# Performance work log

Measured on AMD Instinct MI355X. Metric: run time of the kernel, lower is better.

The kernel has to match this reference:

```python
import jax, jax.numpy as jnp
import numpy as np

LEVELS = (1, 2, 4)
NHEAD = 4
LN_EPS = 1e-5


def _layernorm(x, g, b):
    m = jnp.mean(x, axis=-1, keepdims=True)
    v = jnp.mean((x - m) ** 2, axis=-1, keepdims=True)
    return (x - m) * jax.lax.rsqrt(v + LN_EPS) * g + b


def _spp_pool(x, starts, ends):
    # Exact AdaptiveAvgPool1d over per-proposal segments via inclusive-prefix-sum.
    # x: [B,C,T]; starts/ends: [B,P] int. Returns [B, P, C*sum(LEVELS)].
    B, C, T = x.shape
    P = starts.shape[1]
    xt = jnp.transpose(x, (0, 2, 1))  # [B,T,C]
    csum = jnp.concatenate([jnp.zeros((B, 1, C), x.dtype), jnp.cumsum(xt, axis=1)], axis=1)  # [B,T+1,C]
    n = ends - starts  # [B,P], always >= 1
    feats = []
    for L in LEVELS:
        i = jnp.arange(L)
        lo = (starts[..., None] + (i * n[..., None]) // L).reshape(B, P * L)
        hi = (starts[..., None] + ((i + 1) * n[..., None] + L - 1) // L).reshape(B, P * L)
        slo = jnp.take_along_axis(csum, lo[..., None], axis=1)  # [B,P*L,C]
        shi = jnp.take_along_axis(csum, hi[..., None], axis=1)
        mean = (shi - slo) / (hi - lo).astype(x.dtype)[..., None]
        # torch view(N, C*L) flattens [C,L] C-major -> transpose bins to last axis
        feats.append(mean.reshape(B, P, L, C).transpose(0, 1, 3, 2).reshape(B, P, C * L))
    return jnp.concatenate(feats, axis=-1)


def _encoder_layer(x, qkv_w, qkv_b, out_w, out_b, g1, b1, w1, bb1, w2, bb2, g2, b2):
    # Post-norm nn.TransformerEncoderLayer with exact-erf gelu, dropout=0 (eval)
    B, P, d = x.shape
    dh = d // NHEAD
    qkv = x @ qkv_w.T + qkv_b  # [B,P,3d]
    q, k, v = jnp.split(qkv, 3, axis=-1)
    sh = lambda t: t.reshape(B, P, NHEAD, dh).transpose(0, 2, 1, 3)  # [B,H,P,dh]
    q, k, v = sh(q), sh(k), sh(v)
    scale = 1.0 / float(np.sqrt(dh))
    attn = jax.nn.softmax(jnp.einsum('bhqd,bhkd->bhqk', q, k) * scale, axis=-1)
    o = jnp.einsum('bhqk,bhkd->bhqd', attn, v).transpose(0, 2, 1, 3).reshape(B, P, d)
    o = o @ out_w.T + out_b
    x = _layernorm(x + o, g1, b1)
    h = jax.nn.gelu(x @ w1.T + bb1, approximate=False) @ w2.T + bb2
    return _layernorm(x + h, g2, b2)


def _forward(x, proposal_boxes, proj_w, proj_b, pos_w1, pos_b1, pos_w2, pos_b2,
             qkv_w, qkv_b, out_w, out_b, ln1_g, ln1_b, ff1_w, ff1_b,
             ff2_w, ff2_b, ln2_g, ln2_b, cls_w, cls_b, det_w, det_b):
    B, C, T = x.shape
    P = proposal_boxes.shape[1]
    starts = jnp.clip(proposal_boxes[..., 0], 0, T - 1)
    ends = jnp.clip(proposal_boxes[..., 1], 1, T)
    ends = jnp.where(ends <= starts, jnp.minimum(starts + 1, T), ends)
    feats = _spp_pool(x, starts, ends)  # [B,P,spp_out_dim]
    s_f = proposal_boxes[..., 0].astype(x.dtype)
    e_f = proposal_boxes[..., 1].astype(x.dtype)
    centers = (s_f + e_f) / 2.0
    lengths = jnp.maximum(e_f - s_f, 1.0)
    pos_feat = jnp.stack([centers / T, lengths / T], axis=-1)  # [B,P,2]
    sort_idx = jnp.argsort(centers, axis=1)
    feats_s = jnp.take_along_axis(feats, sort_idx[..., None], axis=1)
    pos_emb = jax.nn.relu(pos_feat @ pos_w1.T + pos_b1) @ pos_w2.T + pos_b2
    pos_emb_s = jnp.take_along_axis(pos_emb, sort_idx[..., None], axis=1)
    tok = feats_s @ proj_w.T + proj_b + pos_emb_s  # [B,P,d]
    for l in range(qkv_w.shape[0]):
        tok = _encoder_layer(tok, qkv_w[l], qkv_b[l], out_w[l], out_b[l],
                             ln1_g[l], ln1_b[l], ff1_w[l], ff1_b[l],
                             ff2_w[l], ff2_b[l], ln2_g[l], ln2_b[l])
    inv = jnp.argsort(sort_idx, axis=1)
    ctx = jnp.take_along_axis(tok, inv[..., None], axis=1)  # [B,P,d]
    class_logits = ctx @ cls_w.T + cls_b  # [B,P,nc]
    det_logits = ctx @ det_w.T + det_b
    class_prob = jax.nn.softmax(class_logits, axis=2)
    det_prob = jax.nn.softmax(det_logits, axis=1)
    joint_prob = class_prob * det_prob
    video_prob = joint_prob.sum(axis=1)
    return video_prob, joint_prob, class_logits, det_logits, ctx


def setup_inputs() -> dict:
    key = jax.random.key(0)
    ks = jax.random.split(key, 32)
    B, C, T, P = 8, 512, 2048, 512
    d, dff, nc, nl = 512, 1024, 30, 2
    spp_out = C * sum(LEVELS)
    s = 0.02
    f32 = jnp.float32
    inp = {
        'x': jax.random.normal(ks[0], (B, C, T), f32),
        'proposal_boxes': jax.random.randint(ks[1], (B, P, 2), 0, T).astype(jnp.int32),
        'proj_w': jax.random.normal(ks[2], (d, spp_out), f32) * s,
        'proj_b': jnp.zeros((d,), f32),
        'pos_w1': jax.random.normal(ks[3], (d, 2), f32) * s,
        'pos_b1': jnp.zeros((d,), f32),
        'pos_w2': jax.random.normal(ks[4], (d, d), f32) * s,
        'pos_b2': jnp.zeros((d,), f32),
        'qkv_w': jax.random.normal(ks[5], (nl, 3 * d, d), f32) * s,
        'qkv_b': jnp.zeros((nl, 3 * d), f32),
        'out_w': jax.random.normal(ks[6], (nl, d, d), f32) * s,
        'out_b': jnp.zeros((nl, d), f32),
        'ln1_g': jnp.ones((nl, d), f32),
        'ln1_b': jnp.zeros((nl, d), f32),
        'ff1_w': jax.random.normal(ks[7], (nl, dff, d), f32) * s,
        'ff1_b': jnp.zeros((nl, dff), f32),
        'ff2_w': jax.random.normal(ks[8], (nl, d, dff), f32) * s,
        'ff2_b': jnp.zeros((nl, d), f32),
        'ln2_g': jnp.ones((nl, d), f32),
        'ln2_b': jnp.zeros((nl, d), f32),
        'cls_w': jax.random.normal(ks[9], (nc, d), f32) * s,
        'cls_b': jnp.zeros((nc,), f32),
        'det_w': jax.random.normal(ks[10], (nc, d), f32) * s,
        'det_b': jnp.zeros((nc,), f32),
    }
    return inp


def reference(x, proposal_boxes, proj_w, proj_b, pos_w1, pos_b1, pos_w2, pos_b2,
              qkv_w, qkv_b, out_w, out_b, ln1_g, ln1_b, ff1_w, ff1_b,
              ff2_w, ff2_b, ln2_g, ln2_b, cls_w, cls_b, det_w, det_b):
    return _forward(x, proposal_boxes, proj_w, proj_b, pos_w1, pos_b1, pos_w2, pos_b2,
                    qkv_w, qkv_b, out_w, out_b, ln1_g, ln1_b, ff1_w, ff1_b,
                    ff2_w, ff2_b, ln2_g, ln2_b, cls_w, cls_b, det_w, det_b)
```

## Files before the change

kernel.cpp:

```cpp
#include <hip/hip_runtime.h>

#define TDIM 2048
#define CDIM 512
#define BDIM 8
#define PDIM 512
#define DMODEL 512
#define NCOUT 30
#define SPPOUT 3584
#define AKDIM 4096

typedef __attribute__((ext_vector_type(8))) short short8;
typedef __attribute__((ext_vector_type(4))) float f32x4;

typedef const __attribute__((address_space(1))) void* as1cv;
typedef __attribute__((address_space(3))) void* as3v;

__device__ __forceinline__ void gl_lds16(const short* g, short* l){
  __builtin_amdgcn_global_load_lds((as1cv)g, (as3v)l, 16, 0, 0);
}

__device__ __forceinline__ short f2b(float f){
  unsigned u = __float_as_uint(f);
  unsigned r = (u + 0x7fffu + ((u >> 16) & 1u)) >> 16;
  return (short)r;
}

__device__ __forceinline__ float waveSum(float v){
#pragma unroll
  for (int o = 32; o > 0; o >>= 1) v += __shfl_xor(v, o);
  return v;
}
__device__ __forceinline__ float waveMax(float v){
#pragma unroll
  for (int o = 32; o > 0; o >>= 1) v = fmaxf(v, __shfl_xor(v, o));
  return v;
}

__global__ void kprep2(const float* __restrict__ pw, const float* __restrict__ pw2,
                       const float* __restrict__ qw, const float* __restrict__ ow,
                       const float* __restrict__ f1, const float* __restrict__ f2,
                       const float* __restrict__ cl, const float* __restrict__ dt,
                       const float* __restrict__ pb, const float* __restrict__ pb2,
                       const float* __restrict__ cb, const float* __restrict__ db,
                       short* __restrict__ Wc, short* __restrict__ Wd,
                       float* __restrict__ bc, float* __restrict__ bh){
  int i = blockIdx.x * 256 + threadIdx.x;
  if (i < 2097152){
    int r = i >> 12, k = i & 4095;
    float v = (k < SPPOUT) ? pw[(size_t)r * SPPOUT + k] : pw2[(size_t)r * DMODEL + (k - SPPOUT)];
    Wc[i] = f2b(v);
  } else if (i < 6322176){
    int j = i - 2097152;
    float v;
    if (j < 1572864) v = qw[j];
    else if (j < 2097152) v = ow[j - 1572864];
    else if (j < 3145728) v = f1[j - 2097152];
    else if (j < 4194304) v = f2[j - 3145728];
    else if (j < 4209664) v = cl[j - 4194304];
    else v = dt[j - 4209664];
    Wd[j] = f2b(v);
  } else {
    int k = i - 6322176;
    if (k < 512) bc[k] = pb[k] + pb2[k];
    else if (k < 572) bh[k - 512] = (k < 542) ? cb[k - 512] : db[k - 542];
  }
}

__global__ void kscan(const float* __restrict__ x, float* __restrict__ W, float* __restrict__ tot){
  int idx = blockIdx.x;
  int b = idx >> 5, rem = idx & 31, ch = rem >> 1, cg = rem & 1;
  int c = cg * 256 + threadIdx.x;
  const float* xp = x + ((size_t)(b * CDIM + c)) * TDIM + ch * 128;
  float* wp = W + ((size_t)b * TDIM + ch * 128) * CDIM + c;
  float run = 0.f;
  for (int tl = 0; tl < 128; tl += 4){
    float4 v = *(const float4*)(xp + tl);
    run += v.x; wp[(size_t)(tl + 0) * CDIM] = run;
    run += v.y; wp[(size_t)(tl + 1) * CDIM] = run;
    run += v.z; wp[(size_t)(tl + 2) * CDIM] = run;
    run += v.w; wp[(size_t)(tl + 3) * CDIM] = run;
  }
  tot[((size_t)b * 16 + ch) * CDIM + c] = run;
}

__global__ void koff(const float* __restrict__ tot, float* __restrict__ off){
  int b = blockIdx.x >> 1, cg = blockIdx.x & 1;
  int c = cg * 256 + threadIdx.x;
  float run = 0.f;
  for (int ch = 0; ch < 16; ++ch){
    off[((size_t)b * 16 + ch) * CDIM + c] = run;
    run += tot[((size_t)b * 16 + ch) * CDIM + c];
  }
}

__global__ void ksort(const int* __restrict__ boxes, int* __restrict__ sidx, float* __restrict__ out){
  __shared__ unsigned key[PDIM];
  int b = blockIdx.x, t = threadIdx.x;
  if (b == 0 && t < 240) out[t] = 0.f;
  int s = boxes[(size_t)(b * PDIM + t) * 2];
  int e = boxes[(size_t)(b * PDIM + t) * 2 + 1];
  key[t] = ((unsigned)(s + e) << 9) | (unsigned)t;
  __syncthreads();
  for (int k = 2; k <= PDIM; k <<= 1){
    for (int j = k >> 1; j > 0; j >>= 1){
      int ixj = t ^ j;
      if (ixj > t){
        unsigned a = key[t], c2 = key[ixj];
        bool up = ((t & k) == 0);
        bool doswap = up ? (a > c2) : (a < c2);
        if (doswap){ key[t] = c2; key[ixj] = a; }
      }
      __syncthreads();
    }
  }
  sidx[b * PDIM + t] = (int)(key[t] & 511u);
}

__global__ void kspp(const float* __restrict__ W, const float* __restrict__ off,
                     const int* __restrict__ boxes, const int* __restrict__ sidx,
                     const float* __restrict__ pw1, const float* __restrict__ pb1,
                     short* __restrict__ A){
  int blk = blockIdx.x;
  int b = blk >> 9, j = blk & 511;
  int p = sidx[b * PDIM + j];
  int s0 = boxes[(size_t)(b * PDIM + p) * 2];
  int e0 = boxes[(size_t)(b * PDIM + p) * 2 + 1];
  int start = min(max(s0, 0), TDIM - 1);
  int end   = min(max(e0, 1), TDIM);
  if (end <= start) end = min(start + 1, TDIM);
  int n = end - start;

  int lo[7], hi[7], cb[7], cl[7];
  {
    const int Ls[3] = {1, 2, 4};
    const int Bo[3] = {0, 512, 1536};
    int q = 0;
    for (int li = 0; li < 3; ++li){
      int L = Ls[li];
      for (int i = 0; i < L; ++i){
        lo[q] = start + (i * n) / L;
        hi[q] = start + ((i + 1) * n + L - 1) / L;
        cb[q] = Bo[li] + i;
        cl[q] = L;
        ++q;
      }
    }
  }
  float s_f = (float)s0, e_f = (float)e0;
  float px = (s_f + e_f) * 0.5f / (float)TDIM;
  float py = fmaxf(e_f - s_f, 1.f) / (float)TDIM;
  short* Ar = A + (size_t)(b * PDIM + j) * AKDIM;
  const float* Wb = W + (size_t)b * TDIM * CDIM;
  const float* ob = off + (size_t)b * 16 * CDIM;
  for (int c = threadIdx.x; c < CDIM; c += 256){
#pragma unroll
    for (int q = 0; q < 7; ++q){
      int l = lo[q], h = hi[q];
      float fl = (l == 0) ? 0.f : (Wb[(size_t)(l - 1) * CDIM + c] + ob[((l - 1) >> 7) * CDIM + c]);
      float fh = Wb[(size_t)(h - 1) * CDIM + c] + ob[((h - 1) >> 7) * CDIM + c];
      Ar[cb[q] + c * cl[q]] = f2b((fh - fl) / (float)(h - l));
    }
    float hv = pw1[c * 2] * px + pw1[c * 2 + 1] * py + pb1[c];
    Ar[SPPOUT + c] = f2b(fmaxf(hv, 0.f));
  }
}

template<int BN, int SWZ = 0>
__global__ __launch_bounds__(256) void gemm_bt(
    int M, int N, int K,
    const short* __restrict__ A, int lda, long long sAb, long long sAh,
    const short* __restrict__ B, int ldb, long long sBb, long long sBh,
    float* __restrict__ Cf, short* __restrict__ Cb, int ldc, long long sCb, long long sCh,
    int hdiv, float alpha,
    const float* __restrict__ bias, const float* __restrict__ resid, int act)
{
  constexpr int JF = BN / 32;
  __shared__ short As[128 * 64];
  __shared__ short Bs[BN * 64];
  int bx = blockIdx.x, by = blockIdx.y, bz = blockIdx.z;
  if constexpr (SWZ){
    int nx = gridDim.x, ny = gridDim.y;
    int rt = ny >> 3;
    int flat = (bz * ny + by) * nx + bx;
    int xcd = flat & 7, wl = flat >> 3;
    by = xcd * rt + wl % rt;
    int rest = wl / rt;
    bx = rest % nx;
    bz = rest / nx;
  }
  int zb = bz / hdiv, zh = bz - zb * hdiv;
  A += (size_t)zb * sAb + (size_t)zh * sAh;
  B += (size_t)zb * sBb + (size_t)zh * sBh;
  size_t coff = (size_t)zb * sCb + (size_t)zh * sCh;
  int rowBase = by * 128, colBase = bx * BN;
  int t = threadIdx.x;
  int lane = t & 63;
  int wave = t >> 6;
  int wm = (wave >> 1) * 64, wn = (wave & 1) * (BN / 2);
  int lm = lane & 15, quad = lane >> 4;
  int srow = t >> 3;
  int skw = ((t & 7) * 8) ^ ((srow & 7) * 8);

  const short* Agp[4];
#pragma unroll
  for (int it = 0; it < 4; ++it)
    Agp[it] = A + (size_t)min(rowBase + srow + it * 32, M - 1) * lda + skw;
  const short* Bgp[JF];
#pragma unroll
  for (int it = 0; it < JF; ++it)
    Bgp[it] = B + (size_t)min(colBase + srow + it * 32, N - 1) * ldb + skw;

  f32x4 zero4 = {0.f, 0.f, 0.f, 0.f};
  f32x4 acc[4][JF];
#pragma unroll
  for (int i = 0; i < 4; ++i)
#pragma unroll
    for (int j = 0; j < JF; ++j) acc[i][j] = zero4;

  int axr = (lm & 7) * 8;
  for (int k0 = 0; k0 < K; k0 += 64){
#pragma unroll
    for (int it = 0; it < 4; ++it) gl_lds16(Agp[it] + k0, As + it * 2048 + t * 8);
#pragma unroll
    for (int it = 0; it < JF; ++it) gl_lds16(Bgp[it] + k0, Bs + it * 2048 + t * 8);
    __syncthreads();
#pragma unroll
    for (int h = 0; h < 2; ++h){
      int koff = (h * 32 + quad * 8) ^ axr;
      short8 af[4], bfr[JF];
#pragma unroll
      for (int i = 0; i < 4; ++i)
        af[i] = *(const short8*)(As + (wm + i * 16 + lm) * 64 + koff);
#pragma unroll
      for (int j = 0; j < JF; ++j)
        bfr[j] = *(const short8*)(Bs + (wn + j * 16 + lm) * 64 + koff);
#pragma unroll
      for (int i = 0; i < 4; ++i)
#pragma unroll
        for (int j = 0; j < JF; ++j)
          acc[i][j] = __builtin_amdgcn_mfma_f32_16x16x32_bf16(af[i], bfr[j], acc[i][j], 0, 0, 0);
    }
    __syncthreads();
  }

#pragma unroll
  for (int i = 0; i < 4; ++i){
#pragma unroll
    for (int j = 0; j < JF; ++j){
#pragma unroll
      for (int r = 0; r < 4; ++r){
        int row = rowBase + wm + i * 16 + quad * 4 + r;
        int col = colBase + wn + j * 16 + lm;
        if (row < M && col < N){
          float v = acc[i][j][r] * alpha;
          if (bias) v += bias[col];
          size_t ci = coff + (size_t)row * ldc + col;
          if (resid) v += resid[ci];
          if (act) v = 0.5f * v * (1.f + erff(v * 0.7071067811865476f));
          if (Cf) Cf[ci] = v;
          if (Cb) Cb[ci] = f2b(v);
        }
      }
    }
  }
}

__global__ void kredG1(const float* __restrict__ part, const float* __restrict__ bias,
                       float* __restrict__ tok, short* __restrict__ tokb){
  int i = blockIdx.x * 256 + threadIdx.x;
  float v = part[i] + part[i + 2097152] + part[i + 4194304] + part[i + 6291456] + bias[i & 511];
  tok[i] = v;
  tokb[i] = f2b(v);
}

__global__ void kvt(const short* __restrict__ qkvb, short* __restrict__ Vt){
  __shared__ short T[32][33];
  int bh = blockIdx.x, pt = blockIdx.y, nt = blockIdx.z;
  int b = bh >> 2, h = bh & 3;
  int tx = threadIdx.x, ty = threadIdx.y;
  const short* src = qkvb + (size_t)(b * 512) * 1536 + 1024 + h * 128;
  int p0 = pt * 32, n0 = nt * 32;
#pragma unroll
  for (int q = 0; q < 4; ++q)
    T[ty * 4 + q][tx] = src[(size_t)(p0 + ty * 4 + q) * 1536 + n0 + tx];
  __syncthreads();
  short* dst = Vt + (size_t)bh * 128 * 512;
#pragma unroll
  for (int q = 0; q < 4; ++q)
    dst[(size_t)(n0 + ty * 4 + q) * 512 + p0 + tx] = T[tx][ty * 4 + q];
}

__global__ __launch_bounds__(256) void kflash(const short* __restrict__ qkvb,
                                              const short* __restrict__ Vt,
                                              short* __restrict__ ob){
  __shared__ float Ofs[4][16][128];
  __shared__ float Ml[4][16], Ll[4][16], Fw[4][16], Linv[16];
  int bid = blockIdx.x;
  int bh = bid & 31, qt = bid >> 5;
  int b = bh >> 2, h = bh & 3;
  int t = threadIdx.x;
  int w = t >> 6, lane = t & 63;
  int lm = lane & 15, quad = lane >> 4;
  const float SL2 = 0.1275174468f;

  const short* qbase = qkvb + (size_t)(b * 512 + qt * 16 + lm) * 1536 + h * 128 + quad * 8;
  short8 qf[4];
#pragma unroll
  for (int s = 0; s < 4; ++s) qf[s] = *(const short8*)(qbase + s * 32);

  const short* kbase = qkvb + (size_t)(b * 512) * 1536 + 512 + h * 128 + quad * 8;
  const short* vbase = Vt + (size_t)bh * 65536 + (size_t)lm * 512 + quad * 8;

  f32x4 zero4 = {0.f, 0.f, 0.f, 0.f};
  f32x4 Of[8];
#pragma unroll
  for (int i = 0; i < 8; ++i) Of[i] = zero4;
  float mrun[4] = {-1e30f, -1e30f, -1e30f, -1e30f};
  float lrun[4] = {0.f, 0.f, 0.f, 0.f};
  short* Pw = (short*)&Ofs[w][0][0];

#pragma unroll
  for (int kt = 0; kt < 2; ++kt){
    int kb = w * 128 + kt * 64;
    f32x4 Sf[4];
#pragma unroll
    for (int j = 0; j < 4; ++j) Sf[j] = zero4;
#pragma unroll
    for (int s = 0; s < 4; ++s){
#pragma unroll
      for (int j = 0; j < 4; ++j){
        short8 kf = *(const short8*)(kbase + (size_t)(kb + j * 16 + lm) * 1536 + s * 32);
        Sf[j] = __builtin_amdgcn_mfma_f32_16x16x32_bf16(qf[s], kf, Sf[j], 0, 0, 0);
      }
    }
    float alpha[4];
#pragma unroll
    for (int r = 0; r < 4; ++r){
      float mx = fmaxf(fmaxf(Sf[0][r], Sf[1][r]), fmaxf(Sf[2][r], Sf[3][r])) * SL2;
#pragma unroll
      for (int o = 1; o < 16; o <<= 1) mx = fmaxf(mx, __shfl_xor(mx, o));
      float mnew = fmaxf(mrun[r], mx);
      alpha[r] = exp2f(mrun[r] - mnew);
      float psum = 0.f;
#pragma unroll
      for (int j = 0; j < 4; ++j){
        float p = exp2f(Sf[j][r] * SL2 - mnew);
        Sf[j][r] = p;
        psum += p;
      }
#pragma unroll
      for (int o = 1; o < 16; o <<= 1) psum += __shfl_xor(psum, o);
      lrun[r] = lrun[r] * alpha[r] + psum;
      mrun[r] = mnew;
    }
#pragma unroll
    for (int i = 0; i < 8; ++i)
#pragma unroll
      for (int r = 0; r < 4; ++r) Of[i][r] *= alpha[r];
#pragma unroll
    for (int j = 0; j < 4; ++j)
#pragma unroll
      for (int r = 0; r < 4; ++r){
        int q = quad * 4 + r;
        int key = j * 16 + lm;
        Pw[q * 64 + (key ^ ((q & 7) * 8))] = f2b(Sf[j][r]);
      }
#pragma unroll
    for (int ts = 0; ts < 2; ++ts){
      short8 pa = *(const short8*)(Pw + lm * 64 + (((ts * 32 + quad * 8) ^ ((lm & 7) * 8))));
#pragma unroll
      for (int jd = 0; jd < 8; ++jd){
        short8 vf = *(const short8*)(vbase + (size_t)(jd * 16) * 512 + kb + ts * 32);
        Of[jd] = __builtin_amdgcn_mfma_f32_16x16x32_bf16(pa, vf, Of[jd], 0, 0, 0);
      }
    }
  }

#pragma unroll
  for (int jd = 0; jd < 8; ++jd)
#pragma unroll
    for (int r = 0; r < 4; ++r)
      Ofs[w][quad * 4 + r][jd * 16 + lm] = Of[jd][r];
  if (lm == 0){
#pragma unroll
    for (int r = 0; r < 4; ++r){
      Ml[w][quad * 4 + r] = mrun[r];
      Ll[w][quad * 4 + r] = lrun[r];
    }
  }
  __syncthreads();

  if (t < 64){
    int wv = t >> 4, row = t & 15;
    float M = fmaxf(fmaxf(Ml[0][row], Ml[1][row]), fmaxf(Ml[2][row], Ml[3][row]));
    Fw[wv][row] = exp2f(Ml[wv][row] - M);
    if (wv == 0){
      float lsum = Ll[0][row] * exp2f(Ml[0][row] - M) + Ll[1][row] * exp2f(Ml[1][row] - M)
                 + Ll[2][row] * exp2f(Ml[2][row] - M) + Ll[3][row] * exp2f(Ml[3][row] - M);
      Linv[row] = 1.f / lsum;
    }
  }
  __syncthreads();

  {
    int row = t >> 4, dbase = (t & 15) * 8;
    float f0 = Fw[0][row], f1 = Fw[1][row], f2v = Fw[2][row], f3 = Fw[3][row];
    float li = Linv[row];
    short* dst = ob + ((size_t)(b * 512 + qt * 16 + row)) * 512 + h * 128 + dbase;
#pragma unroll
    for (int u = 0; u < 8; ++u){
      float v = Ofs[0][row][dbase + u] * f0 + Ofs[1][row][dbase + u] * f1
              + Ofs[2][row][dbase + u] * f2v + Ofs[3][row][dbase + u] * f3;
      dst[u] = f2b(v * li);
    }
  }
}

__global__ void klnR(const float* __restrict__ part, const float* __restrict__ bias,
                     const float* __restrict__ resid,
                     const float* __restrict__ g, const float* __restrict__ bb,
                     float* __restrict__ Yf, short* __restrict__ Yb){
  int row = blockIdx.x, lane = threadIdx.x;
  size_t base = (size_t)row * DMODEL;
  float v[8]; float s = 0.f;
#pragma unroll
  for (int i = 0; i < 8; ++i){
    int c = lane + 64 * i;
    v[i] = part[base + c] + part[base + c + 2097152] + bias[c] + resid[base + c];
    s += v[i];
  }
  s = waveSum(s);
  float m = s * (1.f / DMODEL);
  float q = 0.f;
#pragma unroll
  for (int i = 0; i < 8; ++i){ float d = v[i] - m; q += d * d; }
  q = waveSum(q);
  float inv = rsqrtf(q * (1.f / DMODEL) + 1e-5f);
#pragma unroll
  for (int i = 0; i < 8; ++i){
    int c = lane + 64 * i;
    float o = (v[i] - m) * inv * g[c] + bb[c];
    Yf[base + c] = o;
    Yb[base + c] = f2b(o);
  }
}

__global__ void kdetsm(const float* __restrict__ hd, float* __restrict__ dp){
  int b = blockIdx.x / NCOUT, c = blockIdx.x % NCOUT, lane = threadIdx.x;
  float v[8]; float m = -1e30f;
#pragma unroll
  for (int i = 0; i < 8; ++i){
    v[i] = hd[((size_t)(b * PDIM) + lane + 64 * i) * 60 + 30 + c];
    m = fmaxf(m, v[i]);
  }
  m = waveMax(m);
  float s = 0.f;
#pragma unroll
  for (int i = 0; i < 8; ++i){ v[i] = expf(v[i] - m); s += v[i]; }
  s = waveSum(s);
  float r = 1.f / s;
#pragma unroll
  for (int i = 0; i < 8; ++i)
    dp[((size_t)(b * PDIM) + lane + 64 * i) * NCOUT + c] = v[i] * r;
}

__global__ void kfinal(const float* __restrict__ hd, const float* __restrict__ dps,
                       const float* __restrict__ tok, const int* __restrict__ sidx,
                       float* __restrict__ out){
  int blk = blockIdx.x;
  int b = blk >> 9, j = blk & 511;
  int lane = threadIdx.x;
  int p = sidx[b * PDIM + j];
  float* video = out;
  float* joint = out + 240;
  float* clso  = out + 123120;
  float* deto  = out + 246000;
  float* ctxo  = out + 368880;
  size_t rs60 = (size_t)(b * PDIM + j) * 60;
  size_t rs30 = (size_t)(b * PDIM + j) * NCOUT;
  size_t ro = (size_t)(b * PDIM + p) * NCOUT;
  float lc = (lane < NCOUT) ? hd[rs60 + lane] : -1e30f;
  float m = waveMax(lc);
  float e = (lane < NCOUT) ? expf(lc - m) : 0.f;
  float s = waveSum(e);
  float cp = e / s;
  if (lane < NCOUT){
    float dv  = hd[rs60 + 30 + lane];
    float dpv = dps[rs30 + lane];
    float jp  = cp * dpv;
    clso[ro + lane] = lc;
    deto[ro + lane] = dv;
    joint[ro + lane] = jp;
    atomicAdd(&video[b * NCOUT + lane], jp);
  }
  const float* tr = tok + (size_t)(b * PDIM + j) * DMODEL;
  float* cr = ctxo + (size_t)(b * PDIM + p) * DMODEL;
  for (int c = lane; c < DMODEL; c += 64) cr[c] = tr[c];
}

extern "C" void kernel_launch(void* const* d_in, const int* in_sizes, int n_in,
                              void* d_out, int out_size, void* d_ws, size_t ws_size,
                              hipStream_t stream) {
  const float* x      = (const float*)d_in[0];
  const int*   boxes  = (const int*)d_in[1];
  const float* proj_w = (const float*)d_in[2];
  const float* proj_b = (const float*)d_in[3];
  const float* pos_w1 = (const float*)d_in[4];
  const float* pos_b1 = (const float*)d_in[5];
  const float* pos_w2 = (const float*)d_in[6];
  const float* pos_b2 = (const float*)d_in[7];
  const float* qkv_w  = (const float*)d_in[8];
  const float* qkv_b  = (const float*)d_in[9];
  const float* out_w  = (const float*)d_in[10];
  const float* out_b  = (const float*)d_in[11];
  const float* ln1_g  = (const float*)d_in[12];
  const float* ln1_b  = (const float*)d_in[13];
  const float* ff1_w  = (const float*)d_in[14];
  const float* ff1_b  = (const float*)d_in[15];
  const float* ff2_w  = (const float*)d_in[16];
  const float* ff2_b  = (const float*)d_in[17];
  const float* ln2_g  = (const float*)d_in[18];
  const float* ln2_b  = (const float*)d_in[19];
  const float* cls_w  = (const float*)d_in[20];
  const float* cls_b  = (const float*)d_in[21];
  const float* det_w  = (const float*)d_in[22];
  const float* det_b  = (const float*)d_in[23];
  float* out = (float*)d_out;
  float* ws  = (float*)d_ws;

  const size_t oR1    = 0;
  const size_t oS     = 9437184;
  const size_t oTok   = 22020096;
  const size_t oTokb  = 24117248;
  const size_t oTok2  = 25165824;
  const size_t oTok2b = 27262976;
  const size_t oWcat  = 28311552;
  const size_t oBcat  = 29360128;
  const size_t oWq    = 29360640;
  const size_t oWo    = 30147072;
  const size_t oWf1   = 30409216;
  const size_t oWf2   = 30933504;
  const size_t oWcls  = 31457792;
  const size_t oTot   = 31473152;
  const size_t oOff   = 31538688;
  const size_t oSidx  = 31604224;
  const size_t oBhead = oTot;

  short* Abf   = (short*)(ws + oR1);
  short* qkvb  = (short*)(ws + oR1);
  short* Vt    = (short*)(ws + oR1 + 3145728);
  short* obufb = (short*)(ws + oR1 + 4194304);
  short* hbufb = (short*)(ws + oR1 + 5242880);
  float* headS = ws + oR1 + 7340032;
  float* dpS   = ws + oR1 + 7585792;
  float* csum  = ws + oS;
  float* Cpart = ws + oS;
  float* Cp2   = ws + oS;
  float* tok   = ws + oTok;
  short* tokb  = (short*)(ws + oTokb);
  float* tok2  = ws + oTok2;
  short* tok2b = (short*)(ws + oTok2b);
  short* Wcatb = (short*)(ws + oWcat);
  float* bcat  = ws + oBcat;
  short* Wq    = (short*)(ws + oWq);
  short* Wo    = (short*)(ws + oWo);
  short* Wf1   = (short*)(ws + oWf1);
  short* Wf2   = (short*)(ws + oWf2);
  short* Whead = (short*)(ws + oWcls);
  float* tot   = ws + oTot;
  float* offp  = ws + oOff;
  int*   sidx  = (int*)(ws + oSidx);
  float* bhead = ws + oBhead;

  kscan<<<256, 256, 0, stream>>>(x, csum, tot);
  koff<<<16, 256, 0, stream>>>(tot, offp);
  ksort<<<BDIM, 512, 0, stream>>>(boxes, sidx, out);
  kprep2<<<24699, 256, 0, stream>>>(proj_w, pos_w2, qkv_w, out_w, ff1_w, ff2_w, cls_w, det_w,
                                    proj_b, pos_b2, cls_b, det_b, Wcatb, Wq, bcat, bhead);
  kspp<<<BDIM * PDIM, 256, 0, stream>>>(csum, offp, boxes, sidx, pos_w1, pos_b1, Abf);

  gemm_bt<128, 1><<<dim3(4, 32, 4), 256, 0, stream>>>(
      4096, 512, 1024, Abf, 4096, 1024, 0, Wcatb, 4096, 1024, 0,
      Cpart, nullptr, 512, 2097152, 0, 1, 1.f, nullptr, nullptr, 0);
  kredG1<<<8192, 256, 0, stream>>>(Cpart, bcat, tok, tokb);

  for (int l = 0; l < 2; ++l){
    const short* qw  = Wq  + (size_t)l * 1536 * 512;
    const short* ow  = Wo  + (size_t)l * 512 * 512;
    const short* f1w = Wf1 + (size_t)l * 1024 * 512;
    const short* f2w = Wf2 + (size_t)l * 512 * 1024;
    const float* qb  = qkv_b + (size_t)l * 1536;
    const float* obv = out_b + (size_t)l * 512;
    const float* f1b = ff1_b + (size_t)l * 1024;
    const float* f2b_ = ff2_b + (size_t)l * 512;

    gemm_bt<128, 1><<<dim3(12, 32, 1), 256, 0, stream>>>(
        4096, 1536, 512, tokb, 512, 0, 0, qw, 512, 0, 0,
        nullptr, qkvb, 1536, 0, 0, 1, 1.f, qb, nullptr, 0);
    kvt<<<dim3(32, 16, 4), dim3(32, 8), 0, stream>>>(qkvb, Vt);
    kflash<<<1024, 256, 0, stream>>>(qkvb, Vt, obufb);
    gemm_bt<64><<<dim3(8, 32, 2), 256, 0, stream>>>(
        4096, 512, 256, obufb, 512, 256, 0, ow, 512, 256, 0,
        Cp2, nullptr, 512, 2097152, 0, 1, 1.f, nullptr, nullptr, 0);
    klnR<<<4096, 64, 0, stream>>>(Cp2, obv, tok, ln1_g + l * 512, ln1_b + l * 512, tok2, tok2b);
    gemm_bt<64><<<dim3(16, 32, 1), 256, 0, stream>>>(
        4096, 1024, 512, tok2b, 512, 0, 0, f1w, 512, 0, 0,
        nullptr, hbufb, 1024, 0, 0, 1, 1.f, f1b, nullptr, 1);
    gemm_bt<64><<<dim3(8, 32, 2), 256, 0, stream>>>(
        4096, 512, 512, hbufb, 1024, 512, 0, f2w, 1024, 512, 0,
        Cp2, nullptr, 512, 2097152, 0, 1, 1.f, nullptr, nullptr, 0);
    klnR<<<4096, 64, 0, stream>>>(Cp2, f2b_, tok2, ln2_g + l * 512, ln2_b + l * 512, tok, tokb);
  }

  gemm_bt<64><<<dim3(1, 32, 1), 256, 0, stream>>>(
      4096, 60, 512, tokb, 512, 0, 0, Whead, 512, 0, 0,
      headS, nullptr, 60, 0, 0, 1, 1.f, bhead, nullptr, 0);
  kdetsm<<<BDIM * NCOUT, 64, 0, stream>>>(headS, dpS);
  kfinal<<<BDIM * PDIM, 64, 0, stream>>>(headS, dpS, tok, sidx, out);
}
```

Before: 554.7 us.

## Fuse V transpose into QKV GEMM epilogue and widen split-K for projections

The QKV projection GEMM now writes the V part directly in transposed layout through an LDS staging tile in its epilogue, which removes the separate kvt transpose kernel. The out-projection and FF2 GEMMs go from 2-way to 4-way split-K, and the LayerNorm reduction kernel now sums four partial buffers. Several GEMMs switch to BN=64 tiles with more blocks to raise parallelism. The trade-off is more partial-sum traffic in the reduction kernels and an extra shared-memory pass in the V blocks.

Measured after the change: 522.6 us. 1.06x faster.

```diff
diff --git a/kernel.cpp b/kernel.cpp
--- a/kernel.cpp
+++ b/kernel.cpp
@@ -10,6 +10,7 @@
 #define AKDIM 4096
 
 typedef __attribute__((ext_vector_type(8))) short short8;
+typedef __attribute__((ext_vector_type(4))) short short4v;
 typedef __attribute__((ext_vector_type(4))) float f32x4;
 
 typedef const __attribute__((address_space(1))) void* as1cv;
@@ -172,11 +173,13 @@
     const short* __restrict__ B, int ldb, long long sBb, long long sBh,
     float* __restrict__ Cf, short* __restrict__ Cb, int ldc, long long sCb, long long sCh,
     int hdiv, float alpha,
-    const float* __restrict__ bias, const float* __restrict__ resid, int act)
+    const float* __restrict__ bias, const float* __restrict__ resid, int act,
+    short* __restrict__ Vtp)
 {
   constexpr int JF = BN / 32;
-  __shared__ short As[128 * 64];
-  __shared__ short Bs[BN * 64];
+  __shared__ short smem[128 * 64 + BN * 64];
+  short* As = smem;
+  short* Bs = smem + 128 * 64;
   int bx = blockIdx.x, by = blockIdx.y, bz = blockIdx.z;
   if constexpr (SWZ){
     int nx = gridDim.x, ny = gridDim.y;
@@ -243,6 +246,36 @@
     __syncthreads();
   }
 
+  if (Vtp && colBase >= 1024){
+    short* LT = smem;
+#pragma unroll
+    for (int i = 0; i < 4; ++i){
+#pragma unroll
+      for (int j = 0; j < JF; ++j){
+        int d = wn + j * 16 + lm;
+        int prow = wm + i * 16 + quad * 4;
+        short4v pk;
+#pragma unroll
+        for (int r = 0; r < 4; ++r){
+          float v = acc[i][j][r] * alpha;
+          if (bias) v += bias[colBase + d];
+          pk[r] = f2b(v);
+        }
+        *(short4v*)(LT + d * 132 + prow) = pk;
+      }
+    }
+    __syncthreads();
+    int bb = rowBase >> 9;
+    int hh = (colBase - 1024) >> 7;
+    int dd0 = (colBase - 1024) & 127;
+    int dl = t >> 2, pl = (t & 3) * 32;
+    const short* sp = LT + dl * 132 + pl;
+    short* dp = Vtp + ((size_t)(bb * 4 + hh)) * 65536 + (size_t)(dd0 + dl) * 512 + (rowBase & 511) + pl;
+#pragma unroll
+    for (int u = 0; u < 4; ++u) *(short8*)(dp + u * 8) = *(const short8*)(sp + u * 8);
+    return;
+  }
+
 #pragma unroll
   for (int i = 0; i < 4; ++i){
 #pragma unroll
@@ -273,23 +306,6 @@
   tokb[i] = f2b(v);
 }
 
-__global__ void kvt(const short* __restrict__ qkvb, short* __restrict__ Vt){
-  __shared__ short T[32][33];
-  int bh = blockIdx.x, pt = blockIdx.y, nt = blockIdx.z;
-  int b = bh >> 2, h = bh & 3;
-  int tx = threadIdx.x, ty = threadIdx.y;
-  const short* src = qkvb + (size_t)(b * 512) * 1536 + 1024 + h * 128;
-  int p0 = pt * 32, n0 = nt * 32;
-#pragma unroll
-  for (int q = 0; q < 4; ++q)
-    T[ty * 4 + q][tx] = src[(size_t)(p0 + ty * 4 + q) * 1536 + n0 + tx];
-  __syncthreads();
-  short* dst = Vt + (size_t)bh * 128 * 512;
-#pragma unroll
-  for (int q = 0; q < 4; ++q)
-    dst[(size_t)(n0 + ty * 4 + q) * 512 + p0 + tx] = T[tx][ty * 4 + q];
-}
-
 __global__ __launch_bounds__(256) void kflash(const short* __restrict__ qkvb,
                                               const short* __restrict__ Vt,
                                               short* __restrict__ ob){
@@ -426,7 +442,8 @@
 #pragma unroll
   for (int i = 0; i < 8; ++i){
     int c = lane + 64 * i;
-    v[i] = part[base + c] + part[base + c + 2097152] + bias[c] + resid[base + c];
+    v[i] = part[base + c] + part[base + c + 2097152] + part[base + c + 4194304]
+         + part[base + c + 6291456] + bias[c] + resid[base + c];
     s += v[i];
   }
   s = waveSum(s);
@@ -579,9 +596,9 @@
                                     proj_b, pos_b2, cls_b, det_b, Wcatb, Wq, bcat, bhead);
   kspp<<<BDIM * PDIM, 256, 0, stream>>>(csum, offp, boxes, sidx, pos_w1, pos_b1, Abf);
 
-  gemm_bt<128, 1><<<dim3(4, 32, 4), 256, 0, stream>>>(
+  gemm_bt<64, 1><<<dim3(8, 32, 4), 256, 0, stream>>>(
       4096, 512, 1024, Abf, 4096, 1024, 0, Wcatb, 4096, 1024, 0,
-      Cpart, nullptr, 512, 2097152, 0, 1, 1.f, nullptr, nullptr, 0);
+      Cpart, nullptr, 512, 2097152, 0, 1, 1.f, nullptr, nullptr, 0, nullptr);
   kredG1<<<8192, 256, 0, stream>>>(Cpart, bcat, tok, tokb);
 
   for (int l = 0; l < 2; ++l){
@@ -594,27 +611,26 @@
     const float* f1b = ff1_b + (size_t)l * 1024;
     const float* f2b_ = ff2_b + (size_t)l * 512;
 
-    gemm_bt<128, 1><<<dim3(12, 32, 1), 256, 0, stream>>>(
+    gemm_bt<64><<<dim3(24, 32, 1), 256, 0, stream>>>(
         4096, 1536, 512, tokb, 512, 0, 0, qw, 512, 0, 0,
-        nullptr, qkvb, 1536, 0, 0, 1, 1.f, qb, nullptr, 0);
-    kvt<<<dim3(32, 16, 4), dim3(32, 8), 0, stream>>>(qkvb, Vt);
+        nullptr, qkvb, 1536, 0, 0, 1, 1.f, qb, nullptr, 0, Vt);
     kflash<<<1024, 256, 0, stream>>>(qkvb, Vt, obufb);
-    gemm_bt<64><<<dim3(8, 32, 2), 256, 0, stream>>>(
-        4096, 512, 256, obufb, 512, 256, 0, ow, 512, 256, 0,
-        Cp2, nullptr, 512, 2097152, 0, 1, 1.f, nullptr, nullptr, 0);
+    gemm_bt<64><<<dim3(8, 32, 4), 256, 0, stream>>>(
+        4096, 512, 128, obufb, 512, 128, 0, ow, 512, 128, 0,
+        Cp2, nullptr, 512, 2097152, 0, 1, 1.f, nullptr, nullptr, 0, nullptr);
     klnR<<<4096, 64, 0, stream>>>(Cp2, obv, tok, ln1_g + l * 512, ln1_b + l * 512, tok2, tok2b);
     gemm_bt<64><<<dim3(16, 32, 1), 256, 0, stream>>>(
         4096, 1024, 512, tok2b, 512, 0, 0, f1w, 512, 0, 0,
-        nullptr, hbufb, 1024, 0, 0, 1, 1.f, f1b, nullptr, 1);
-    gemm_bt<64><<<dim3(8, 32, 2), 256, 0, stream>>>(
-        4096, 512, 512, hbufb, 1024, 512, 0, f2w, 1024, 512, 0,
-        Cp2, nullptr, 512, 2097152, 0, 1, 1.f, nullptr, nullptr, 0);
+        nullptr, hbufb, 1024, 0, 0, 1, 1.f, f1b, nullptr, 1, nullptr);
+    gemm_bt<64><<<dim3(8, 32, 4), 256, 0, stream>>>(
+        4096, 512, 256, hbufb, 1024, 256, 0, f2w, 1024, 256, 0,
+        Cp2, nullptr, 512, 2097152, 0, 1, 1.f, nullptr, nullptr, 0, nullptr);
     klnR<<<4096, 64, 0, stream>>>(Cp2, f2b_, tok2, ln2_g + l * 512, ln2_b + l * 512, tok, tokb);
   }
 
   gemm_bt<64><<<dim3(1, 32, 1), 256, 0, stream>>>(
       4096, 60, 512, tokb, 512, 0, 0, Whead, 512, 0, 0,
-      headS, nullptr, 60, 0, 0, 1, 1.f, bhead, nullptr, 0);
+      headS, nullptr, 60, 0, 0, 1, 1.f, bhead, nullptr, 0, nullptr);
   kdetsm<<<BDIM * NCOUT, 64, 0, stream>>>(headS, dpS);
   kfinal<<<BDIM * PDIM, 64, 0, stream>>>(headS, dpS, tok, sidx, out);
 }
```
